# Optimization experiments

Measured on AMD Instinct MI355X. Metric: run time of the kernel, lower is better.

The kernel has to match this reference:

```python
import jax, jax.numpy as jnp
import numpy as np

DIM = 512
NUM_HEADS = 8


def setup_inputs() -> dict:
    key = jax.random.key(0)
    ks = jax.random.split(key, 9)
    B, C, H, W = 8, DIM, 32, 32
    s = 1.0 / np.sqrt(DIM)  # conv-style init scale
    return {
        "x": jax.random.normal(ks[0], (B, C, H, W), jnp.float32),
        "Wq": jax.random.normal(ks[1], (DIM, DIM), jnp.float32) * s,
        "bq": jnp.zeros((DIM,), jnp.float32),
        "Wk": jax.random.normal(ks[2], (DIM, DIM), jnp.float32) * s,
        "bk": jnp.zeros((DIM,), jnp.float32),
        "Wv": jax.random.normal(ks[3], (DIM, DIM), jnp.float32) * s,
        "bv": jnp.zeros((DIM,), jnp.float32),
        "Wo": jax.random.normal(ks[4], (DIM, DIM), jnp.float32) * s,
        "bo": jnp.zeros((DIM,), jnp.float32),
    }


def _proj(x, W, b):
    # 1x1 conv == per-pixel linear over channels: [out_c, in_c] x [b, in_c, h, w]
    return jnp.einsum('oc,bchw->bohw', W, x) + b[None, :, None, None]


def reference(x, Wq, bq, Wk, bk, Wv, bv, Wo, bo):
    b, c, h, w = x.shape
    g = NUM_HEADS
    dh = c // g  # per-head channels
    q = _proj(x, Wq, bq)
    k = _proj(x, Wk, bk)
    v = _proj(x, Wv, bv)
    # 'b (g c) h w -> (b g) c (h w)'
    def split_heads(t):
        return t.reshape(b, g, dh, h * w).reshape(b * g, dh, h * w)
    q, k, v = split_heads(q), split_heads(k), split_heads(v)
    # note: scale uses full dim (as in the source), not per-head dim
    a = jnp.einsum('bcs,bct->bst', q, k) / jnp.sqrt(jnp.float32(c))
    a = jax.nn.softmax(a, axis=-1)  # dropout is identity at inference
    o = jnp.einsum('bst,bct->bcs', a, v)  # [(b g), dh, s]
    o = o.reshape(b, g * dh, h, w)  # '(b g) c (h w) -> b (g c) h w'
    return x + _proj(o, Wo, bo)
```

## Files before the change

### kernel.cpp

```cpp
#include <hip/hip_runtime.h>

typedef unsigned short u16;
typedef __attribute__((ext_vector_type(8))) short short8;
typedef __attribute__((ext_vector_type(4))) short sh4;
typedef __attribute__((ext_vector_type(2))) int int2v;
typedef __attribute__((ext_vector_type(4))) float floatx4;

__device__ __forceinline__ float b2f(u16 u) {
  unsigned int x = ((unsigned int)u) << 16;
  return __builtin_bit_cast(float, x);
}
__device__ __forceinline__ u16 f2b(float f) {
  unsigned int x = __builtin_bit_cast(unsigned int, f);
  unsigned int r = (x + 0x7FFFu + ((x >> 16) & 1u)) >> 16;
  return (u16)r;
}
__device__ __forceinline__ unsigned int pk2bf(float a, float b) {
  unsigned int ua = __builtin_bit_cast(unsigned int, a) + 0x8000u;
  unsigned int ub = __builtin_bit_cast(unsigned int, b) + 0x8000u;
  return __builtin_amdgcn_perm(ub, ua, 0x07060302u);
}

#if __has_builtin(__builtin_amdgcn_mfma_f32_16x16x16bf16_1k)
#define MFMA16(a, b, c) __builtin_amdgcn_mfma_f32_16x16x16bf16_1k((a), (b), (c), 0, 0, 0)
#define MFMA16_DRAIN()
#else
__device__ __forceinline__ floatx4 mfma16_fb(sh4 a, sh4 b, floatx4 c) {
  asm volatile("s_nop 1\n\tv_mfma_f32_16x16x16_bf16 %0, %1, %2, %0"
               : "+v"(c) : "v"(a), "v"(b));
  return c;
}
#define MFMA16(a, b, c) mfma16_fb((a), (b), (c))
#define MFMA16_DRAIN() asm volatile("s_nop 7\n\ts_nop 7\n\ts_nop 7")
#endif

#if __has_builtin(__builtin_amdgcn_exp2f)
#define EXP2F(x) __builtin_amdgcn_exp2f(x)
#else
#define EXP2F(x) __expf((x) * 0.6931471805599453f)
#endif

#define MFMA32(a, b, c) __builtin_amdgcn_mfma_f32_16x16x32_bf16((a), (b), (c), 0, 0, 0)

#define GLL16(g, l) __builtin_amdgcn_global_load_lds(                         \
    (const __attribute__((address_space(1))) unsigned int*)(g),               \
    (__attribute__((address_space(3))) unsigned int*)(l), 16, 0, 0)

#define SC_LOG2E 0.06375872f

__device__ __forceinline__ int detect_fp32(const u16* __restrict__ x) {
  __shared__ int cnt;
  if (threadIdx.x == 0) cnt = 0;
  __syncthreads();
  int c = 0;
  if (threadIdx.x < 256) {
#pragma unroll
    for (int i = 0; i < 16; ++i) {
      u16 u = x[threadIdx.x * 16 + i];
      if (((u >> 7) & 0xFF) >= 0xC8) c++;
    }
  }
  if (c) atomicAdd(&cnt, c);
  __syncthreads();
  return cnt > 32;
}

__global__ __launch_bounds__(256) void prep(
    const u16* __restrict__ x,
    const u16* w0, const u16* w1, const u16* w2, const u16* w3,
    const u16* c0, const u16* c1, const u16* c2, const u16* c3,
    u16* __restrict__ xT, u16* __restrict__ Wc, u16* __restrict__ bc, int b0) {
  const int fp32 = detect_fp32(x);
  const int tid = threadIdx.x;
  if (blockIdx.y < 8) {
    __shared__ u16 t[64][65];
    const int lb = blockIdx.z, b = b0 + lb;
    const int p0 = blockIdx.x * 64, cc0 = blockIdx.y * 64;
    const int tx = tid & 63, ty = tid >> 6;
    if (fp32) {
      const float* xb = (const float*)x + (long)b * 524288;
#pragma unroll
      for (int i = 0; i < 16; ++i) {
        int c = ty + i * 4;
        t[c][tx] = f2b(xb[(long)(cc0 + c) * 1024 + p0 + tx]);
      }
    } else {
      const u16* xb = x + (long)b * 524288;
#pragma unroll
      for (int i = 0; i < 16; ++i) {
        int c = ty + i * 4;
        t[c][tx] = xb[(long)(cc0 + c) * 1024 + p0 + tx];
      }
    }
    __syncthreads();
    u16* xTb = xT + (long)lb * 524288;
#pragma unroll
    for (int i = 0; i < 16; ++i) {
      int p = ty + i * 4;
      xTb[(long)(p0 + p) * 512 + cc0 + tx] = t[tx][p];
    }
  } else {
    const u16* srcs[8] = {w0, w1, w2, w3, c0, c1, c2, c3};
    const int nthreads = gridDim.z * 16 * 256;
    const int flat = (blockIdx.z * 16 + blockIdx.x) * 256 + tid;
    for (int vi = flat; vi < 131072; vi += nthreads) {
      int w = vi >> 15;
      int off = (vi & 32767) * 8;
      u16* dst = Wc + w * 262144 + off;
      if (fp32) {
        const float* s = (const float*)srcs[w] + off;
        u16 tmp[8];
#pragma unroll
        for (int r = 0; r < 8; ++r) tmp[r] = f2b(s[r]);
        *(int4*)dst = *(const int4*)tmp;
      } else {
        *(int4*)dst = *(const int4*)(srcs[w] + off);
      }
    }
    for (int gi = flat; gi < 2048; gi += nthreads) {
      int t2 = gi >> 9;
      bc[gi] = fp32 ? f2b(((const float*)srcs[4 + t2])[gi & 511]) : srcs[4 + t2][gi & 511];
    }
  }
}

struct GemmLdsP {
  u16 As[2][128][32], Bs[2][128][32];
};

__device__ __forceinline__ void gemm_stage(const u16* __restrict__ A, int lda,
                                           const u16* __restrict__ B, int ldb,
                                           int m0, int n0, int k0, int buf,
                                           GemmLdsP& lds) {
  const int tid = threadIdx.x;
  const int wave = tid >> 6, lane = tid & 63;
  const int lrow = lane >> 2, lcol = (lane & 3) * 8;
#pragma unroll
  for (int it = 0; it < 2; ++it) {
    const int rbase = wave * 32 + it * 16;
    GLL16(A + (long)(m0 + rbase + lrow) * lda + k0 + lcol, &lds.As[buf][rbase][0]);
    GLL16(B + (long)(n0 + rbase + lrow) * ldb + k0 + lcol, &lds.Bs[buf][rbase][0]);
  }
}

__device__ __forceinline__ void gemm_core_pipe(const u16* __restrict__ A, int lda,
                                               const u16* __restrict__ B, int ldb,
                                               int m0, int n0, int K,
                                               GemmLdsP& lds, floatx4 (&acc)[4][4]) {
  const int tid = threadIdx.x;
  const int wave = tid >> 6, lane = tid & 63;
  const int quad = lane >> 4, l15 = lane & 15;
  const int wm = (wave >> 1) * 64, wn = (wave & 1) * 64;

  gemm_stage(A, lda, B, ldb, m0, n0, 0, 0, lds);
  __syncthreads();
  for (int k0 = 0; k0 < K; k0 += 32) {
    const int buf = (k0 >> 5) & 1;
    if (k0 + 32 < K) gemm_stage(A, lda, B, ldb, m0, n0, k0 + 32, buf ^ 1, lds);
    short8 af[4], bf[4];
#pragma unroll
    for (int i = 0; i < 4; ++i)
      af[i] = *(const short8*)&lds.As[buf][wm + i * 16 + l15][quad * 8];
#pragma unroll
    for (int j = 0; j < 4; ++j)
      bf[j] = *(const short8*)&lds.Bs[buf][wn + j * 16 + l15][quad * 8];
#pragma unroll
    for (int i = 0; i < 4; ++i)
#pragma unroll
      for (int j = 0; j < 4; ++j)
        acc[i][j] = MFMA32(af[i], bf[j], acc[i][j]);
    __syncthreads();
  }
}

__global__ __launch_bounds__(256) void gemm_qkv(
    const u16* __restrict__ xT, const u16* __restrict__ Wc,
    const u16* __restrict__ bc, u16* __restrict__ Qt, u16* __restrict__ Kt,
    u16* __restrict__ Vv) {
  __shared__ GemmLdsP lds;
  const long bz = blockIdx.x;
  const u16* xb = xT + bz * 524288;
  const int bx = blockIdx.y;
  const int qk = bx < 64;
  const int t = qk ? bx : bx - 64;
  const int m0 = (t >> 3) * 128, n0 = (t & 7) * 128;
  const u16* A = qk ? xb : (Wc + 524288);
  const u16* B = qk ? Wc : xb;
  floatx4 acc[4][4] = {};
  gemm_core_pipe(A, 512, B, 512, m0, n0, 512, lds, acc);
  const int lane = threadIdx.x & 63, wave = threadIdx.x >> 6;
  const int quad = lane >> 4, l15 = lane & 15;
  const int wm = (wave >> 1) * 64, wn = (wave & 1) * 64;
  if (qk) {
    u16* Qz = Qt + bz * 524288;
    u16* Kz = Kt + bz * 524288;
#pragma unroll
    for (int i = 0; i < 4; ++i)
#pragma unroll
      for (int j = 0; j < 4; ++j)
#pragma unroll
        for (int r = 0; r < 4; ++r) {
          int gm = m0 + wm + i * 16 + quad * 4 + r;
          int gn = n0 + wn + j * 16 + l15;
          float v = acc[i][j][r] + b2f(bc[gn]);
          if (gn < 512) Qz[(long)gm * 512 + gn] = f2b(v * SC_LOG2E);
          else Kz[(long)gm * 512 + gn - 512] = f2b(v);
        }
  } else {
    u16* Vz = Vv + bz * 524288;
    const u16* bv = bc + 1024;
#pragma unroll
    for (int i = 0; i < 4; ++i)
#pragma unroll
      for (int j = 0; j < 4; ++j)
#pragma unroll
        for (int r = 0; r < 4; ++r) {
          int gm = m0 + wm + i * 16 + quad * 4 + r;
          int gn = n0 + wn + j * 16 + l15;
          float v = acc[i][j][r] + b2f(bv[gm]);
          Vz[(long)gm * 1024 + gn] = f2b(v);
        }
  }
}

struct OutLdsP {
  u16 As[2][128][32], Bs[2][64][32];
};

__global__ __launch_bounds__(256) void gemm_out(
    const u16* __restrict__ Wo, const u16* __restrict__ bo,
    const u16* __restrict__ Ow, const u16* __restrict__ xraw,
    u16* __restrict__ out) {
  const int fp32 = detect_fp32(xraw);
  __shared__ OutLdsP lds;
  const long bz = blockIdx.x;
  const u16* B = Ow + bz * 524288;
  const int m0 = blockIdx.z * 128, n0 = blockIdx.y * 64;
  const int tid = threadIdx.x;
  const int wave = tid >> 6, lane = tid & 63;
  const int quad = lane >> 4, l15 = lane & 15;
  const int lrow = lane >> 2, lcol = (lane & 3) * 8;

  floatx4 acc[2][4] = {};

#define OUT_STAGE(buf, k0)                                                    \
  {                                                                           \
    const int ra = wave * 32;                                                 \
    GLL16(Wo + (long)(m0 + ra + lrow) * 512 + (k0) + lcol,                    \
          &lds.As[buf][ra][0]);                                               \
    GLL16(Wo + (long)(m0 + ra + 16 + lrow) * 512 + (k0) + lcol,               \
          &lds.As[buf][ra + 16][0]);                                          \
    GLL16(B + (long)(n0 + wave * 16 + lrow) * 512 + (k0) + lcol,              \
          &lds.Bs[buf][wave * 16][0]);                                        \
  }

  OUT_STAGE(0, 0);
  __syncthreads();
  for (int k0 = 0; k0 < 512; k0 += 32) {
    const int buf = (k0 >> 5) & 1;
    if (k0 + 32 < 512) OUT_STAGE(buf ^ 1, k0 + 32);
#pragma unroll
    for (int i = 0; i < 2; ++i) {
      short8 af = *(const short8*)&lds.As[buf][wave * 32 + i * 16 + l15][quad * 8];
#pragma unroll
      for (int j = 0; j < 4; ++j) {
        short8 bf = *(const short8*)&lds.Bs[buf][j * 16 + l15][quad * 8];
        acc[i][j] = MFMA32(af, bf, acc[i][j]);
      }
    }
    __syncthreads();
  }
#undef OUT_STAGE

#pragma unroll
  for (int i = 0; i < 2; ++i)
#pragma unroll
    for (int j = 0; j < 4; ++j)
#pragma unroll
      for (int r = 0; r < 4; ++r) {
        int gm = m0 + wave * 32 + i * 16 + quad * 4 + r;
        int gn = n0 + j * 16 + l15;
        float v = acc[i][j][r] + b2f(bo[gm]);
        long idx = bz * 524288 + (long)gm * 1024 + gn;
        if (fp32) {
          v += ((const float*)xraw)[idx];
          ((float*)out)[idx] = v;
        } else {
          v += b2f(xraw[idx]);
          out[idx] = f2b(v);
        }
      }
}

#define AP 72
__global__ __launch_bounds__(256, 2) void attn(
    const u16* __restrict__ Qt, const u16* __restrict__ Kt,
    const u16* __restrict__ V, u16* __restrict__ O) {
  __shared__ alignas(16) u16 Ks[2][64][AP];
  __shared__ alignas(16) u16 Vs[2][64][AP];
  const int bg = blockIdx.x;
  const int lb = bg >> 3, head = bg & 7;
  const int s0 = blockIdx.y * 128;
  const int tid = threadIdx.x;
  const int wave = tid >> 6, lane = tid & 63;
  const int quad = lane >> 4, l15 = lane & 15;

  const u16* Qb = Qt + (long)lb * 524288 + head * 64;
  const u16* Kb = Kt + (long)lb * 524288 + head * 64;
  const u16* Vb = V + (long)(lb * 512 + head * 64) * 1024;
  u16* Ob = O + (long)lb * 524288 + head * 64;

  short8 bq[2][2];
#pragma unroll
  for (int qb = 0; qb < 2; ++qb)
#pragma unroll
    for (int kk = 0; kk < 2; ++kk)
      bq[qb][kk] = *(const short8*)&Qb[(long)(s0 + wave * 32 + qb * 16 + l15) * 512 +
                                       kk * 32 + quad * 8];

  const int r0 = tid >> 3, o0 = (tid & 7) * 8;
  int4 kreg0, kreg1, vreg0, vreg1;
  kreg0 = *(const int4*)&Kb[(long)r0 * 512 + o0];
  kreg1 = *(const int4*)&Kb[(long)(r0 + 32) * 512 + o0];
  vreg0 = *(const int4*)&Vb[(long)r0 * 1024 + o0];
  vreg1 = *(const int4*)&Vb[(long)(r0 + 32) * 1024 + o0];
  *(int4*)&Ks[0][r0][o0] = kreg0;
  *(int4*)&Ks[0][r0 + 32][o0] = kreg1;
  *(int4*)&Vs[0][r0][o0] = vreg0;
  *(int4*)&Vs[0][r0 + 32][o0] = vreg1;

  floatx4 acc[2][4] = {};
  floatx4 accl[2] = {};
  const sh4 ones = {(short)0x3F80, (short)0x3F80, (short)0x3F80, (short)0x3F80};

  for (int it16 = 0; it16 < 16; ++it16) {
    const int buf = it16 & 1;
    const int t0n = (it16 + 1) * 64;
    if (it16 < 15) {
      kreg0 = *(const int4*)&Kb[(long)(t0n + r0) * 512 + o0];
      kreg1 = *(const int4*)&Kb[(long)(t0n + r0 + 32) * 512 + o0];
      vreg0 = *(const int4*)&Vb[(long)r0 * 1024 + t0n + o0];
      vreg1 = *(const int4*)&Vb[(long)(r0 + 32) * 1024 + t0n + o0];
    }
    __syncthreads();

    floatx4 p[2][4] = {};
#pragma unroll
    for (int kk = 0; kk < 2; ++kk) {
      short8 ak[4];
#pragma unroll
      for (int mi = 0; mi < 4; ++mi)
        ak[mi] = *(const short8*)&Ks[buf][mi * 16 + l15][kk * 32 + quad * 8];
#pragma unroll
      for (int qb = 0; qb < 2; ++qb)
#pragma unroll
        for (int mi = 0; mi < 4; ++mi)
          p[qb][mi] = MFMA32(ak[mi], bq[qb][kk], p[qb][mi]);
    }

    sh4 pk[2][4];
#pragma unroll
    for (int qb = 0; qb < 2; ++qb)
#pragma unroll
      for (int mi = 0; mi < 4; ++mi) {
        float e0 = EXP2F(p[qb][mi][0]);
        float e1 = EXP2F(p[qb][mi][1]);
        float e2 = EXP2F(p[qb][mi][2]);
        float e3 = EXP2F(p[qb][mi][3]);
        int2v w;
        w.x = (int)pk2bf(e0, e1);
        w.y = (int)pk2bf(e2, e3);
        pk[qb][mi] = __builtin_bit_cast(sh4, w);
      }

#pragma unroll
    for (int qb = 0; qb < 2; ++qb)
#pragma unroll
      for (int mi = 0; mi < 4; ++mi) accl[qb] = MFMA16(ones, pk[qb][mi], accl[qb]);

#pragma unroll
    for (int mi = 0; mi < 4; ++mi) {
      sh4 av[4];
#pragma unroll
      for (int ci = 0; ci < 4; ++ci)
        av[ci] = *(const sh4*)&Vs[buf][ci * 16 + l15][mi * 16 + quad * 4];
#pragma unroll
      for (int qb = 0; qb < 2; ++qb)
#pragma unroll
        for (int ci = 0; ci < 4; ++ci)
          acc[qb][ci] = MFMA16(av[ci], pk[qb][mi], acc[qb][ci]);
    }

    if (it16 < 15) {
      const int nb = 1 - buf;
      *(int4*)&Ks[nb][r0][o0] = kreg0;
      *(int4*)&Ks[nb][r0 + 32][o0] = kreg1;
      *(int4*)&Vs[nb][r0][o0] = vreg0;
      *(int4*)&Vs[nb][r0 + 32][o0] = vreg1;
    }
  }
  MFMA16_DRAIN();

  const float inv0 = 1.0f / accl[0][0];
  const float inv1 = 1.0f / accl[1][0];

  u16 (*Os)[AP] = (u16(*)[AP]) & Ks[0][0][0];
  __syncthreads();
#pragma unroll
  for (int qb = 0; qb < 2; ++qb) {
    const float inv = qb ? inv1 : inv0;
#pragma unroll
    for (int ci = 0; ci < 4; ++ci) {
      int2v w;
      w.x = (int)pk2bf(acc[qb][ci][0] * inv, acc[qb][ci][1] * inv);
      w.y = (int)pk2bf(acc[qb][ci][2] * inv, acc[qb][ci][3] * inv);
      *(int2v*)&Os[wave * 32 + qb * 16 + l15][ci * 16 + quad * 4] = w;
    }
  }
  __syncthreads();
  {
    const int srow = tid >> 1, cb = (tid & 1) * 32;
#pragma unroll
    for (int c = 0; c < 32; c += 8)
      *(int4*)&Ob[(long)(s0 + srow) * 512 + cb + c] = *(const int4*)&Os[srow][cb + c];
  }
}

extern "C" void kernel_launch(void* const* d_in, const int* in_sizes, int n_in,
                              void* d_out, int out_size, void* d_ws, size_t ws_size,
                              hipStream_t stream) {
  const u16* x  = (const u16*)d_in[0];
  const u16* Wq = (const u16*)d_in[1];
  const u16* bq = (const u16*)d_in[2];
  const u16* Wk = (const u16*)d_in[3];
  const u16* bk = (const u16*)d_in[4];
  const u16* Wv = (const u16*)d_in[5];
  const u16* bv = (const u16*)d_in[6];
  const u16* Wo = (const u16*)d_in[7];
  const u16* bo = (const u16*)d_in[8];
  u16* out = (u16*)d_out;
  u16* ws = (u16*)d_ws;

  const size_t PLAN_A_BYTES = 27267072;

  if (ws_size >= PLAN_A_BYTES) {
    u16* xT = ws;
    u16* Kt = ws + 4194304;
    u16* Vv = ws + 8388608;
    u16* Wc = ws + 12582912;
    u16* bc = ws + 13631488;
    u16* Qt = out;
    u16* Ow = xT;

    prep<<<dim3(16, 9, 8), 256, 0, stream>>>(x, Wq, Wk, Wv, Wo,
                                             bq, bk, bv, bo, xT, Wc, bc, 0);
    gemm_qkv<<<dim3(8, 96), 256, 0, stream>>>(xT, Wc, bc, Qt, Kt, Vv);
    attn<<<dim3(64, 8), 256, 0, stream>>>(Qt, Kt, Vv, Ow);
    gemm_out<<<dim3(8, 16, 4), 256, 0, stream>>>(Wc + 786432, bc + 1536, Ow, x, out);
  } else {
    u16* Ow = ws;
    u16* Kt = ws + 4194304;
    u16* Vv = ws + 6291456;
    u16* Wc = ws + 8388608;
    u16* bc = ws + 9437184;
    u16* Qt = out;

    for (int phase = 0; phase < 2; ++phase) {
      const int b0 = phase * 4;
      u16* xT = Ow + (long)phase * 2097152;
      prep<<<dim3(16, 9, 4), 256, 0, stream>>>(x, Wq, Wk, Wv, Wo,
                                               bq, bk, bv, bo, xT, Wc, bc, b0);
      gemm_qkv<<<dim3(4, 96), 256, 0, stream>>>(xT, Wc, bc, Qt, Kt, Vv);
      attn<<<dim3(32, 8), 256, 0, stream>>>(Qt, Kt, Vv, Ow + (long)b0 * 524288);
    }
    gemm_out<<<dim3(8, 16, 4), 256, 0, stream>>>(Wc + 786432, bc + 1536, Ow, x, out);
  }
}
```

Measured before the change: 158.8 us.

## Triple-buffer LDS in QKV and output GEMMs with one barrier per k-step

Both GEMM kernels move from double to triple LDS buffers. Each k-step now issues the next stage's async loads, waits on vmcnt only for the current stage, and runs a single s_barrier instead of two __syncthreads. The aim is fewer barrier stalls and more overlap between global-to-LDS loads and MFMA work. The cost is more LDS per block (48KB for QKV), which may reduce occupancy, and hand-written vmcnt counts that must stay in step with the number of loads per stage.

```diff
diff --git a/kernel.cpp b/kernel.cpp
--- a/kernel.cpp
+++ b/kernel.cpp
@@ -124,14 +124,14 @@
   }
 }
 
-struct GemmLdsP {
-  u16 As[2][128][32], Bs[2][128][32];
+struct GemmLds3 {
+  u16 As[3][128][32], Bs[3][128][32];
 };
 
-__device__ __forceinline__ void gemm_stage(const u16* __restrict__ A, int lda,
-                                           const u16* __restrict__ B, int ldb,
-                                           int m0, int n0, int k0, int buf,
-                                           GemmLdsP& lds) {
+__device__ __forceinline__ void gemm_stage3(const u16* __restrict__ A, int lda,
+                                            const u16* __restrict__ B, int ldb,
+                                            int m0, int n0, int k0, int buf,
+                                            GemmLds3& lds) {
   const int tid = threadIdx.x;
   const int wave = tid >> 6, lane = tid & 63;
   const int lrow = lane >> 2, lcol = (lane & 3) * 8;
@@ -143,33 +143,40 @@
   }
 }
 
-__device__ __forceinline__ void gemm_core_pipe(const u16* __restrict__ A, int lda,
-                                               const u16* __restrict__ B, int ldb,
-                                               int m0, int n0, int K,
-                                               GemmLdsP& lds, floatx4 (&acc)[4][4]) {
+__device__ __forceinline__ void gemm_core_pipe3(const u16* __restrict__ A, int lda,
+                                                const u16* __restrict__ B, int ldb,
+                                                int m0, int n0,
+                                                GemmLds3& lds, floatx4 (&acc)[4][4]) {
   const int tid = threadIdx.x;
   const int wave = tid >> 6, lane = tid & 63;
   const int quad = lane >> 4, l15 = lane & 15;
   const int wm = (wave >> 1) * 64, wn = (wave & 1) * 64;
 
-  gemm_stage(A, lda, B, ldb, m0, n0, 0, 0, lds);
-  __syncthreads();
-  for (int k0 = 0; k0 < K; k0 += 32) {
-    const int buf = (k0 >> 5) & 1;
-    if (k0 + 32 < K) gemm_stage(A, lda, B, ldb, m0, n0, k0 + 32, buf ^ 1, lds);
+  gemm_stage3(A, lda, B, ldb, m0, n0, 0, 0, lds);
+  int buf = 0, nbuf = 1;
+  for (int i = 0; i < 16; ++i) {
+    if (i < 15) {
+      gemm_stage3(A, lda, B, ldb, m0, n0, (i + 1) * 32, nbuf, lds);
+      asm volatile("s_waitcnt vmcnt(4)" ::: "memory");
+    } else {
+      asm volatile("s_waitcnt vmcnt(0)" ::: "memory");
+    }
+    __builtin_amdgcn_s_barrier();
+    __builtin_amdgcn_sched_barrier(0);
     short8 af[4], bf[4];
 #pragma unroll
-    for (int i = 0; i < 4; ++i)
-      af[i] = *(const short8*)&lds.As[buf][wm + i * 16 + l15][quad * 8];
+    for (int ii = 0; ii < 4; ++ii)
+      af[ii] = *(const short8*)&lds.As[buf][wm + ii * 16 + l15][quad * 8];
 #pragma unroll
     for (int j = 0; j < 4; ++j)
       bf[j] = *(const short8*)&lds.Bs[buf][wn + j * 16 + l15][quad * 8];
 #pragma unroll
-    for (int i = 0; i < 4; ++i)
+    for (int ii = 0; ii < 4; ++ii)
 #pragma unroll
       for (int j = 0; j < 4; ++j)
-        acc[i][j] = MFMA32(af[i], bf[j], acc[i][j]);
-    __syncthreads();
+        acc[ii][j] = MFMA32(af[ii], bf[j], acc[ii][j]);
+    buf = nbuf;
+    nbuf = nbuf == 2 ? 0 : nbuf + 1;
   }
 }
 
@@ -177,7 +184,7 @@
     const u16* __restrict__ xT, const u16* __restrict__ Wc,
     const u16* __restrict__ bc, u16* __restrict__ Qt, u16* __restrict__ Kt,
     u16* __restrict__ Vv) {
-  __shared__ GemmLdsP lds;
+  __shared__ GemmLds3 lds;
   const long bz = blockIdx.x;
   const u16* xb = xT + bz * 524288;
   const int bx = blockIdx.y;
@@ -187,7 +194,7 @@
   const u16* A = qk ? xb : (Wc + 524288);
   const u16* B = qk ? Wc : xb;
   floatx4 acc[4][4] = {};
-  gemm_core_pipe(A, 512, B, 512, m0, n0, 512, lds, acc);
+  gemm_core_pipe3(A, 512, B, 512, m0, n0, lds, acc);
   const int lane = threadIdx.x & 63, wave = threadIdx.x >> 6;
   const int quad = lane >> 4, l15 = lane & 15;
   const int wm = (wave >> 1) * 64, wn = (wave & 1) * 64;
@@ -223,8 +230,8 @@
   }
 }
 
-struct OutLdsP {
-  u16 As[2][128][32], Bs[2][64][32];
+struct OutLds3 {
+  u16 As[3][128][32], Bs[3][64][32];
 };
 
 __global__ __launch_bounds__(256) void gemm_out(
@@ -232,7 +239,7 @@
     const u16* __restrict__ Ow, const u16* __restrict__ xraw,
     u16* __restrict__ out) {
   const int fp32 = detect_fp32(xraw);
-  __shared__ OutLdsP lds;
+  __shared__ OutLds3 lds;
   const long bz = blockIdx.x;
   const u16* B = Ow + bz * 524288;
   const int m0 = blockIdx.z * 128, n0 = blockIdx.y * 64;
@@ -243,34 +250,41 @@
 
   floatx4 acc[2][4] = {};
 
-#define OUT_STAGE(buf, k0)                                                    \
+#define OUT_STAGE3(bufi, k0)                                                  \
   {                                                                           \
     const int ra = wave * 32;                                                 \
     GLL16(Wo + (long)(m0 + ra + lrow) * 512 + (k0) + lcol,                    \
-          &lds.As[buf][ra][0]);                                               \
+          &lds.As[bufi][ra][0]);                                              \
     GLL16(Wo + (long)(m0 + ra + 16 + lrow) * 512 + (k0) + lcol,               \
-          &lds.As[buf][ra + 16][0]);                                          \
+          &lds.As[bufi][ra + 16][0]);                                         \
     GLL16(B + (long)(n0 + wave * 16 + lrow) * 512 + (k0) + lcol,              \
-          &lds.Bs[buf][wave * 16][0]);                                        \
-  }
-
-  OUT_STAGE(0, 0);
-  __syncthreads();
-  for (int k0 = 0; k0 < 512; k0 += 32) {
-    const int buf = (k0 >> 5) & 1;
-    if (k0 + 32 < 512) OUT_STAGE(buf ^ 1, k0 + 32);
-#pragma unroll
-    for (int i = 0; i < 2; ++i) {
-      short8 af = *(const short8*)&lds.As[buf][wave * 32 + i * 16 + l15][quad * 8];
+          &lds.Bs[bufi][wave * 16][0]);                                       \
+  }
+
+  OUT_STAGE3(0, 0);
+  int buf = 0, nbuf = 1;
+  for (int i = 0; i < 16; ++i) {
+    if (i < 15) {
+      OUT_STAGE3(nbuf, (i + 1) * 32);
+      asm volatile("s_waitcnt vmcnt(3)" ::: "memory");
+    } else {
+      asm volatile("s_waitcnt vmcnt(0)" ::: "memory");
+    }
+    __builtin_amdgcn_s_barrier();
+    __builtin_amdgcn_sched_barrier(0);
+#pragma unroll
+    for (int ii = 0; ii < 2; ++ii) {
+      short8 af = *(const short8*)&lds.As[buf][wave * 32 + ii * 16 + l15][quad * 8];
 #pragma unroll
       for (int j = 0; j < 4; ++j) {
         short8 bf = *(const short8*)&lds.Bs[buf][j * 16 + l15][quad * 8];
-        acc[i][j] = MFMA32(af, bf, acc[i][j]);
-      }
-    }
-    __syncthreads();
-  }
-#undef OUT_STAGE
+        acc[ii][j] = MFMA32(af, bf, acc[ii][j]);
+      }
+    }
+    buf = nbuf;
+    nbuf = nbuf == 2 ? 0 : nbuf + 1;
+  }
+#undef OUT_STAGE3
 
 #pragma unroll
   for (int i = 0; i < 2; ++i)
```

Measured after the change: 155.7 us, median of 2. Within noise of the previous version (-1.9%).
